# Kernel optimization log

Hardware: AMD Instinct MI355X
Metric: run time of the kernel (lower is better)

The kernel has to match this reference:

```python
import jax, jax.numpy as jnp
import numpy as np

N_NODES = 50000
NEG_SLOPE = 0.2  # PyG GATConv default
DROP_P = 0.3


def gat_layer(x, src, dst, W, a_src, a_dst, b, n):
    # x: [N, din]; src/dst: [E'] (self-loops already appended)
    h = x @ W                                   # [N, dout]
    s_src = (h * a_src).sum(-1)                 # [N]
    s_dst = (h * a_dst).sum(-1)                 # [N]
    alpha = jax.nn.leaky_relu(s_src[src] + s_dst[dst], NEG_SLOPE)  # [E']
    # segment softmax over destination node
    amax = jax.ops.segment_max(alpha, dst, num_segments=n)
    e = jnp.exp(alpha - amax[dst])
    denom = jax.ops.segment_sum(e, dst, num_segments=n)
    coef = e / denom[dst]                       # [E']
    out = jax.ops.segment_sum(coef[:, None] * h[src], dst, num_segments=n)
    return out + b


def setup_inputs() -> dict:
    key = jax.random.key(0)
    ks = jax.random.split(key, 10)
    d1, d2 = 64, 64
    E = jax.random.normal(ks[0], (N_NODES, d1), jnp.float32)
    A = jax.random.randint(ks[1], (2, 800000), 0, N_NODES, jnp.int64)
    W1 = jax.random.normal(ks[2], (d1, d1), jnp.float32) / np.sqrt(d1)
    a_src1 = jax.random.normal(ks[3], (d1,), jnp.float32) / np.sqrt(d1)
    a_dst1 = jax.random.normal(ks[4], (d1,), jnp.float32) / np.sqrt(d1)
    b1 = jnp.zeros((d1,), jnp.float32)
    W2 = jax.random.normal(ks[5], (d1, d2), jnp.float32) / np.sqrt(d1)
    a_src2 = jax.random.normal(ks[6], (d2,), jnp.float32) / np.sqrt(d2)
    a_dst2 = jax.random.normal(ks[7], (d2,), jnp.float32) / np.sqrt(d2)
    b2 = jnp.zeros((d2,), jnp.float32)
    return {"E": E, "A": A, "W1": W1, "a_src1": a_src1, "a_dst1": a_dst1,
            "b1": b1, "W2": W2, "a_src2": a_src2, "a_dst2": a_dst2, "b2": b2}


def reference(E, A, W1, a_src1, a_dst1, b1, W2, a_src2, a_dst2, b2):
    n = E.shape[0]
    loop = jnp.arange(n, dtype=A.dtype)
    src = jnp.concatenate([A[0], loop])  # PyG GATConv adds self-loops
    dst = jnp.concatenate([A[1], loop])
    x1 = jax.nn.relu(gat_layer(E, src, dst, W1, a_src1, a_dst1, b1, n))
    # F.dropout(p=0.3) runs in training mode by default -> deterministic fixed-key mask
    keep = jax.random.bernoulli(jax.random.key(42), 1.0 - DROP_P, x1.shape)
    x1 = jnp.where(keep, x1 / (1.0 - DROP_P), 0.0)
    x2 = jax.nn.relu(gat_layer(x1, src, dst, W2, a_src2, a_dst2, b2, n))
    return x2
```

## Files before the change

### kernel.cpp

```cpp
#include <hip/hip_runtime.h>


__device__ __forceinline__ unsigned rotl32(unsigned x, unsigned r) {
  return (x << r) | (x >> (32u - r));
}

__device__ __forceinline__ void threefry2_0_42(unsigned c0, unsigned c1,
                                               unsigned* o0, unsigned* o1) {
  const unsigned k0 = 0u, k1 = 42u;
  const unsigned k2 = k0 ^ k1 ^ 0x1BD11BDAu;
  unsigned ks[3] = {k0, k1, k2};
  unsigned x0 = c0 + ks[0];
  unsigned x1 = c1 + ks[1];
  const unsigned R[2][4] = {{13u, 15u, 26u, 6u}, {17u, 29u, 16u, 24u}};
#pragma unroll
  for (int i = 0; i < 5; ++i) {
#pragma unroll
    for (int j = 0; j < 4; ++j) {
      unsigned r = R[i & 1][j];
      x0 += x1;
      x1 = rotl32(x1, r);
      x1 ^= x0;
    }
    x0 += ks[(i + 1) % 3];
    x1 += ks[(i + 2) % 3] + (unsigned)(i + 1);
  }
  *o0 = x0;
  *o1 = x1;
}

__device__ __forceinline__ float ldf(const void* p, int isbf, size_t i) {
  if (isbf) {
    unsigned short u = ((const unsigned short*)p)[i];
    return __uint_as_float(((unsigned)u) << 16);
  }
  return ((const float*)p)[i];
}

__global__ __launch_bounds__(256) void k_prep(
    const void* __restrict__ A, const void* __restrict__ Ein, int nNodes,
    const void* W1, const void* as1, const void* ad1, const void* b1,
    const void* W2, const void* as2, const void* ad2, const void* b2,
    float* __restrict__ smallc, int* __restrict__ deg, int* __restrict__ cursor,
    int* __restrict__ flags) {
  __shared__ int s_ok64, s_bf;
  int t = threadIdx.x;
  if (t == 0) { s_ok64 = 1; s_bf = 0; }
  __syncthreads();
  long long v = ((const long long*)A)[t];
  if (!(v >= 0 && v < (long long)nNodes)) atomicAnd(&s_ok64, 0);
  unsigned w = ((const unsigned*)Ein)[t];
  unsigned b = (w >> 8) & 0x7F;
  if (b >= 0x3A && b <= 0x43) atomicAdd(&s_bf, 1);
  __syncthreads();
  int isbf = (s_bf >= 200) ? 1 : 0;
  int i = blockIdx.x * 256 + t;
  if (blockIdx.x == 0 && t == 0) {
    flags[0] = s_ok64;
    flags[1] = isbf;
  }
  if (i < 8576) {
    float x;
    if (i < 4096) x = ldf(W1, isbf, i);
    else if (i < 4160) x = ldf(as1, isbf, i - 4096);
    else if (i < 4224) x = ldf(ad1, isbf, i - 4160);
    else if (i < 4288) x = ldf(b1, isbf, i - 4224);
    else if (i < 8384) x = ldf(W2, isbf, i - 4288);
    else if (i < 8448) x = ldf(as2, isbf, i - 8384);
    else if (i < 8512) x = ldf(ad2, isbf, i - 8448);
    else x = ldf(b2, isbf, i - 8512);
    smallc[i] = x;
  }
  if (i < nNodes) {
    deg[i] = 1;
    cursor[i] = 0;
  }
}

__global__ __launch_bounds__(256) void k_count_gemm(
    const void* __restrict__ A, const int* __restrict__ flags, int Eb,
    int* __restrict__ deg, const void* __restrict__ X,
    const float* __restrict__ W, const float* __restrict__ a_src,
    const float* __restrict__ a_dst, float* __restrict__ H,
    float* __restrict__ ssrc, float* __restrict__ sdst, int n,
    int nCountBlocks) {
  __shared__ float Wl[64 * 64];
  int t = threadIdx.x;
  if ((int)blockIdx.x < nCountBlocks) {
    int e = blockIdx.x * 256 + t;
    if (e < Eb) {
      int d = flags[0] ? (int)((const long long*)A)[(long long)Eb + e]
                       : ((const int*)A)[Eb + e];
      atomicAdd(&deg[d], 1);
    }
    return;
  }
  int bid = blockIdx.x - nCountBlocks;
  for (int i = t; i < 64 * 64; i += 256) Wl[i] = W[i];
  __syncthreads();
  int lane = t & 63;
  int row = bid * 4 + (t >> 6);
  if (row >= n) return;
  int isbf = flags[1];
  float xv = ldf(X, isbf, (size_t)row * 64 + lane);
  float acc = 0.f;
#pragma unroll
  for (int k = 0; k < 64; ++k) {
    float xk = __shfl(xv, k);
    acc = fmaf(xk, Wl[k * 64 + lane], acc);
  }
  H[(size_t)row * 64 + lane] = acc;
  float vs = acc * a_src[lane];
  float vd = acc * a_dst[lane];
#pragma unroll
  for (int d = 32; d; d >>= 1) {
    vs += __shfl_xor(vs, d);
    vd += __shfl_xor(vd, d);
  }
  if (lane == 0) {
    ssrc[row] = vs;
    sdst[row] = vd;
  }
}

__global__ __launch_bounds__(256) void k_gemm64(
    const float* __restrict__ X, const float* __restrict__ W,
    const float* __restrict__ a_src, const float* __restrict__ a_dst,
    float* __restrict__ H, float* __restrict__ ssrc, float* __restrict__ sdst,
    int n) {
  __shared__ float Wl[64 * 64];
  int t = threadIdx.x;
  for (int i = t; i < 64 * 64; i += 256) Wl[i] = W[i];
  __syncthreads();
  int lane = t & 63;
  int row = blockIdx.x * 4 + (t >> 6);
  if (row >= n) return;
  float xv = X[(size_t)row * 64 + lane];
  float acc = 0.f;
#pragma unroll
  for (int k = 0; k < 64; ++k) {
    float xk = __shfl(xv, k);
    acc = fmaf(xk, Wl[k * 64 + lane], acc);
  }
  H[(size_t)row * 64 + lane] = acc;
  float vs = acc * a_src[lane];
  float vd = acc * a_dst[lane];
#pragma unroll
  for (int d = 32; d; d >>= 1) {
    vs += __shfl_xor(vs, d);
    vd += __shfl_xor(vd, d);
  }
  if (lane == 0) {
    ssrc[row] = vs;
    sdst[row] = vd;
  }
}

__global__ __launch_bounds__(1024) void k_scan_one(const int* __restrict__ deg,
                                                   int* __restrict__ offsets,
                                                   int n, int etot) {
  __shared__ int wsum[16];
  __shared__ int carry;
  int t = threadIdx.x;
  int lane = t & 63;
  int w = t >> 6;
  if (t == 0) carry = 0;
  __syncthreads();
  for (int base = 0; base < n; base += 1024) {
    int i = base + t;
    int x = (i < n) ? deg[i] : 0;
    int sc = x;
#pragma unroll
    for (int d = 1; d < 64; d <<= 1) {
      int o = __shfl_up(sc, d);
      if (lane >= d) sc += o;
    }
    if (lane == 63) wsum[w] = sc;
    __syncthreads();
    int cbase = carry;
    if (t < 64) {
      int v = (t < 16) ? wsum[t] : 0;
#pragma unroll
      for (int d = 1; d < 16; d <<= 1) {
        int o = __shfl_up(v, d);
        if (lane >= d) v += o;
      }
      if (t < 16) wsum[t] = v;
    }
    __syncthreads();
    int wpre = (w == 0) ? 0 : wsum[w - 1];
    if (i < n) offsets[i] = cbase + wpre + (sc - x);
    int tot = wsum[15];
    __syncthreads();
    if (t == 0) carry = cbase + tot;
    __syncthreads();
  }
  if (t == 0) offsets[n] = etot;
}

__global__ __launch_bounds__(256) void k_fill(const void* __restrict__ A,
                                              const int* __restrict__ flags,
                                              const int* __restrict__ offsets,
                                              int* cursor, int* __restrict__ csr,
                                              int Eb, int nnode) {
  int e = blockIdx.x * 256 + threadIdx.x;
  if (e >= Eb + nnode) return;
  int s, d;
  if (e < Eb) {
    if (flags[0]) {
      s = (int)((const long long*)A)[e];
      d = (int)((const long long*)A)[(long long)Eb + e];
    } else {
      s = ((const int*)A)[e];
      d = ((const int*)A)[Eb + e];
    }
  } else {
    s = d = e - Eb;
  }
  int slot = atomicAdd(&cursor[d], 1);
  csr[offsets[d] + slot] = s;
}

#define AGG_STEP(IDX, ACC)                                              \
  {                                                                     \
    int idx_ = (IDX);                                                   \
    float cl_ = __shfl(c, idx_);                                        \
    int sr_ = __shfl(sl, idx_);                                         \
    if (idx_ < glim) {                                                  \
      const float4 hv_ = *(const float4*)&h[(size_t)sr_ * 64 + f4 * 4]; \
      ACC.x = fmaf(cl_, hv_.x, ACC.x);                                  \
      ACC.y = fmaf(cl_, hv_.y, ACC.y);                                  \
      ACC.z = fmaf(cl_, hv_.z, ACC.z);                                  \
      ACC.w = fmaf(cl_, hv_.w, ACC.w);                                  \
    }                                                                   \
  }

template <int DROPOUT>
__global__ __launch_bounds__(256) void k_aggregate(
    const float* __restrict__ h, const float* __restrict__ ssrc,
    const float* __restrict__ sdst, const float* __restrict__ bias,
    const int* __restrict__ offsets, const int* __restrict__ csr,
    float* __restrict__ alphaE, float* __restrict__ out, int n) {
  int wid = (blockIdx.x * 256 + threadIdx.x) >> 6;
  int lane = threadIdx.x & 63;
  if (wid >= n) return;
  int off = offsets[wid];
  int end = offsets[wid + 1];
  int g = end - off;
  float sd = sdst[wid];
  int e4 = lane >> 4, f4 = lane & 15;
  float4 acc0 = {0.f, 0.f, 0.f, 0.f}, acc1 = {0.f, 0.f, 0.f, 0.f};

  if (g <= 64) {
    int sl = 0;
    float v = -1e30f;
    if (lane < g) {
      sl = csr[off + lane];
      float tv = ssrc[sl] + sd;
      v = (tv > 0.f) ? tv : 0.2f * tv;
    }
    float m = v;
#pragma unroll
    for (int d = 32; d; d >>= 1) m = fmaxf(m, __shfl_xor(m, d));
    float ex = (lane < g) ? __expf(v - m) : 0.f;
    float s = ex;
#pragma unroll
    for (int d = 32; d; d >>= 1) s += __shfl_xor(s, d);
    float c = ex * (1.f / s);
    int glim = g;
    for (int cb = 0; cb < g; cb += 8) {
      AGG_STEP(cb + e4, acc0)
      AGG_STEP(cb + 4 + e4, acc1)
    }
  } else {
    float mm = -1e30f, ss = 0.f;
    for (int e = off + lane; e < end; e += 64) {
      int sl2 = csr[e];
      float tv = ssrc[sl2] + sd;
      tv = (tv > 0.f) ? tv : 0.2f * tv;
      alphaE[e] = tv;
      float mn = fmaxf(mm, tv);
      ss = ss * __expf(mm - mn) + __expf(tv - mn);
      mm = mn;
    }
#pragma unroll
    for (int d = 32; d; d >>= 1) {
      float mo = __shfl_xor(mm, d);
      float so = __shfl_xor(ss, d);
      float mn = fmaxf(mm, mo);
      ss = ss * __expf(mm - mn) + so * __expf(mo - mn);
      mm = mn;
    }
    float inv = 1.f / ss;
    for (int base = off; base < end; base += 64) {
      int e = base + lane;
      int cnt = min(64, end - base);
      float c = 0.f;
      int sl = 0;
      if (e < end) {
        c = __expf(alphaE[e] - mm) * inv;
        sl = csr[e];
      }
      int glim = cnt;
      for (int cb = 0; cb < cnt; cb += 8) {
        AGG_STEP(cb + e4, acc0)
        AGG_STEP(cb + 4 + e4, acc1)
      }
    }
  }

  float4 r;
  r.x = acc0.x + acc1.x;
  r.y = acc0.y + acc1.y;
  r.z = acc0.z + acc1.z;
  r.w = acc0.w + acc1.w;
#pragma unroll
  for (int d = 16; d < 64; d <<= 1) {
    r.x += __shfl_xor(r.x, d);
    r.y += __shfl_xor(r.y, d);
    r.z += __shfl_xor(r.z, d);
    r.w += __shfl_xor(r.w, d);
  }

  unsigned long long mask = 0ull;
  if (DROPOUT) {
    unsigned i0 = (unsigned)wid * 64u + (unsigned)lane;
    unsigned o0, o1;
    threefry2_0_42(0u, i0, &o0, &o1);
    unsigned bits = o0 ^ o1;
    float u = __uint_as_float((bits >> 9) | 0x3f800000u) - 1.0f;
    mask = __ballot(u < 0.7f);
  }

  if (lane < 16) {
    const float4 b4 = *(const float4*)&bias[lane * 4];
    r.x = fmaxf(r.x + b4.x, 0.f);
    r.y = fmaxf(r.y + b4.y, 0.f);
    r.z = fmaxf(r.z + b4.z, 0.f);
    r.w = fmaxf(r.w + b4.w, 0.f);
    if (DROPOUT) {
      r.x = ((mask >> (lane * 4 + 0)) & 1ull) ? r.x / 0.7f : 0.f;
      r.y = ((mask >> (lane * 4 + 1)) & 1ull) ? r.y / 0.7f : 0.f;
      r.z = ((mask >> (lane * 4 + 2)) & 1ull) ? r.z / 0.7f : 0.f;
      r.w = ((mask >> (lane * 4 + 3)) & 1ull) ? r.w / 0.7f : 0.f;
    }
    *(float4*)&out[(size_t)wid * 64 + lane * 4] = r;
  }
}

extern "C" void kernel_launch(void* const* d_in, const int* in_sizes, int n_in,
                              void* d_out, int out_size, void* d_ws, size_t ws_size,
                              hipStream_t stream) {
  const void* E = d_in[0];
  const void* A = d_in[1];
  const void* W1 = d_in[2];
  const void* as1 = d_in[3];
  const void* ad1 = d_in[4];
  const void* b1 = d_in[5];
  const void* W2 = d_in[6];
  const void* as2 = d_in[7];
  const void* ad2 = d_in[8];
  const void* b2 = d_in[9];
  float* out = (float*)d_out;

  const int N = in_sizes[0] / 64;
  const int Eb = in_sizes[1] / 2;
  const int Etot = Eb + N;
  const int total = N * 64;

  float* ws = (float*)d_ws;
  float* h = ws;
  float* x1 = h + (size_t)total;
  float* ssrc = x1 + (size_t)total;
  float* sdst = ssrc + N;
  float* alphaE = sdst + N;
  float* smallc = alphaE + Etot;
  int* deg = (int*)(smallc + 8576);
  int* offsets = deg + N;
  int* cursor = offsets + (N + 1);
  int* flags = cursor + N;
  int* csr = flags + 2;

  float* W1c = smallc;
  float* as1c = smallc + 4096;
  float* ad1c = smallc + 4160;
  float* b1c = smallc + 4224;
  float* W2c = smallc + 4288;
  float* as2c = smallc + 8384;
  float* ad2c = smallc + 8448;
  float* b2c = smallc + 8512;

  const int gPrep = (N + 255) / 256;
  const int nCountBlocks = (Eb + 255) / 256;
  const int gGemm = (N + 3) / 4;
  const int gFill = (Etot + 255) / 256;

  k_prep<<<gPrep, 256, 0, stream>>>(A, E, N, W1, as1, ad1, b1, W2, as2, ad2,
                                    b2, smallc, deg, cursor, flags);
  k_count_gemm<<<nCountBlocks + gGemm, 256, 0, stream>>>(
      A, flags, Eb, deg, E, W1c, as1c, ad1c, h, ssrc, sdst, N, nCountBlocks);
  k_scan_one<<<1, 1024, 0, stream>>>(deg, offsets, N, Etot);
  k_fill<<<gFill, 256, 0, stream>>>(A, flags, offsets, cursor, csr, Eb, N);
  k_aggregate<1><<<gGemm, 256, 0, stream>>>(h, ssrc, sdst, b1c, offsets, csr,
                                            alphaE, x1, N);
  k_gemm64<<<gGemm, 256, 0, stream>>>(x1, W2c, as2c, ad2c, h, ssrc, sdst, N);
  k_aggregate<0><<<gGemm, 256, 0, stream>>>(h, ssrc, sdst, b2c, offsets, csr,
                                            alphaE, out, N);
}
```

Before: 396.4 us.

## Use register-tiled 64x64 GEMM with transposed X in shared memory

Replaces the per-row shuffle-based GEMM, one wavefront per row, with a 64-row tile per block. X is staged transposed in padded LDS and each thread computes a 4x4 output block using float4 loads from shared memory. The attention scores are reduced with 16-lane shuffles. The separate second-layer GEMM kernel is removed, and the second layer reuses the combined kernel with zero count blocks. This cuts shared-memory traffic per FMA and raises arithmetic intensity, at the cost of more LDS per block and a transposed scatter on load.

```diff
diff --git a/kernel.cpp b/kernel.cpp
--- a/kernel.cpp
+++ b/kernel.cpp
@@ -1,5 +1,7 @@
 #include <hip/hip_runtime.h>
 
+
+#define XT_STRIDE 68
 
 __device__ __forceinline__ unsigned rotl32(unsigned x, unsigned r) {
   return (x << r) | (x >> (32u - r));
@@ -79,12 +81,13 @@
 
 __global__ __launch_bounds__(256) void k_count_gemm(
     const void* __restrict__ A, const int* __restrict__ flags, int Eb,
-    int* __restrict__ deg, const void* __restrict__ X,
+    int* __restrict__ deg, const void* __restrict__ X, int xDetect,
     const float* __restrict__ W, const float* __restrict__ a_src,
     const float* __restrict__ a_dst, float* __restrict__ H,
     float* __restrict__ ssrc, float* __restrict__ sdst, int n,
     int nCountBlocks) {
-  __shared__ float Wl[64 * 64];
+  __shared__ float Xt[64 * XT_STRIDE];
+  __shared__ float Ws[64 * 64];
   int t = threadIdx.x;
   if ((int)blockIdx.x < nCountBlocks) {
     int e = blockIdx.x * 256 + t;
@@ -96,63 +99,83 @@
     return;
   }
   int bid = blockIdx.x - nCountBlocks;
-  for (int i = t; i < 64 * 64; i += 256) Wl[i] = W[i];
+  int row0 = bid * 64;
+  int isbf = xDetect ? flags[1] : 0;
+
+#pragma unroll
+  for (int i = t; i < 1024; i += 256) {
+    int k = i >> 4, jq = i & 15;
+    *(float4*)&Ws[k * 64 + jq * 4] = *(const float4*)&W[k * 64 + jq * 4];
+  }
+#pragma unroll
+  for (int i = t; i < 1024; i += 256) {
+    int q = i & 15, r = i >> 4;
+    int row = row0 + r;
+    float4 v = {0.f, 0.f, 0.f, 0.f};
+    if (row < n) {
+      if (isbf) {
+        v.x = ldf(X, 1, (size_t)row * 64 + q * 4 + 0);
+        v.y = ldf(X, 1, (size_t)row * 64 + q * 4 + 1);
+        v.z = ldf(X, 1, (size_t)row * 64 + q * 4 + 2);
+        v.w = ldf(X, 1, (size_t)row * 64 + q * 4 + 3);
+      } else {
+        v = *(const float4*)&((const float*)X)[(size_t)row * 64 + q * 4];
+      }
+    }
+    Xt[(q * 4 + 0) * XT_STRIDE + r] = v.x;
+    Xt[(q * 4 + 1) * XT_STRIDE + r] = v.y;
+    Xt[(q * 4 + 2) * XT_STRIDE + r] = v.z;
+    Xt[(q * 4 + 3) * XT_STRIDE + r] = v.w;
+  }
   __syncthreads();
-  int lane = t & 63;
-  int row = bid * 4 + (t >> 6);
-  if (row >= n) return;
-  int isbf = flags[1];
-  float xv = ldf(X, isbf, (size_t)row * 64 + lane);
-  float acc = 0.f;
-#pragma unroll
+
+  int r0 = (t >> 4) * 4;
+  int c0 = (t & 15) * 4;
+  float acc[4][4];
+#pragma unroll
+  for (int r = 0; r < 4; ++r)
+#pragma unroll
+    for (int c = 0; c < 4; ++c) acc[r][c] = 0.f;
+
+#pragma unroll 8
   for (int k = 0; k < 64; ++k) {
-    float xk = __shfl(xv, k);
-    acc = fmaf(xk, Wl[k * 64 + lane], acc);
-  }
-  H[(size_t)row * 64 + lane] = acc;
-  float vs = acc * a_src[lane];
-  float vd = acc * a_dst[lane];
-#pragma unroll
-  for (int d = 32; d; d >>= 1) {
-    vs += __shfl_xor(vs, d);
-    vd += __shfl_xor(vd, d);
-  }
-  if (lane == 0) {
-    ssrc[row] = vs;
-    sdst[row] = vd;
-  }
-}
-
-__global__ __launch_bounds__(256) void k_gemm64(
-    const float* __restrict__ X, const float* __restrict__ W,
-    const float* __restrict__ a_src, const float* __restrict__ a_dst,
-    float* __restrict__ H, float* __restrict__ ssrc, float* __restrict__ sdst,
-    int n) {
-  __shared__ float Wl[64 * 64];
-  int t = threadIdx.x;
-  for (int i = t; i < 64 * 64; i += 256) Wl[i] = W[i];
-  __syncthreads();
-  int lane = t & 63;
-  int row = blockIdx.x * 4 + (t >> 6);
-  if (row >= n) return;
-  float xv = X[(size_t)row * 64 + lane];
-  float acc = 0.f;
-#pragma unroll
-  for (int k = 0; k < 64; ++k) {
-    float xk = __shfl(xv, k);
-    acc = fmaf(xk, Wl[k * 64 + lane], acc);
-  }
-  H[(size_t)row * 64 + lane] = acc;
-  float vs = acc * a_src[lane];
-  float vd = acc * a_dst[lane];
-#pragma unroll
-  for (int d = 32; d; d >>= 1) {
-    vs += __shfl_xor(vs, d);
-    vd += __shfl_xor(vd, d);
-  }
-  if (lane == 0) {
-    ssrc[row] = vs;
-    sdst[row] = vd;
+    float4 a4 = *(const float4*)&Xt[k * XT_STRIDE + r0];
+    float4 b4 = *(const float4*)&Ws[k * 64 + c0];
+    const float av[4] = {a4.x, a4.y, a4.z, a4.w};
+    const float bv[4] = {b4.x, b4.y, b4.z, b4.w};
+#pragma unroll
+    for (int r = 0; r < 4; ++r)
+#pragma unroll
+      for (int c = 0; c < 4; ++c) acc[r][c] = fmaf(av[r], bv[c], acc[r][c]);
+  }
+
+  const float4 asr = *(const float4*)&a_src[c0];
+  const float4 adr = *(const float4*)&a_dst[c0];
+#pragma unroll
+  for (int r = 0; r < 4; ++r) {
+    float vs = acc[r][0] * asr.x + acc[r][1] * asr.y + acc[r][2] * asr.z +
+               acc[r][3] * asr.w;
+    float vd = acc[r][0] * adr.x + acc[r][1] * adr.y + acc[r][2] * adr.z +
+               acc[r][3] * adr.w;
+#pragma unroll
+    for (int d = 1; d < 16; d <<= 1) {
+      vs += __shfl_xor(vs, d);
+      vd += __shfl_xor(vd, d);
+    }
+    int row = row0 + r0 + r;
+    if ((t & 15) == 0 && row < n) {
+      ssrc[row] = vs;
+      sdst[row] = vd;
+    }
+  }
+
+#pragma unroll
+  for (int r = 0; r < 4; ++r) {
+    int row = row0 + r0 + r;
+    if (row < n) {
+      float4 o = {acc[r][0], acc[r][1], acc[r][2], acc[r][3]};
+      *(float4*)&H[(size_t)row * 64 + c0] = o;
+    }
   }
 }
 
@@ -392,18 +415,20 @@
 
   const int gPrep = (N + 255) / 256;
   const int nCountBlocks = (Eb + 255) / 256;
-  const int gGemm = (N + 3) / 4;
+  const int gTile = (N + 63) / 64;
+  const int gAgg = (N + 3) / 4;
   const int gFill = (Etot + 255) / 256;
 
   k_prep<<<gPrep, 256, 0, stream>>>(A, E, N, W1, as1, ad1, b1, W2, as2, ad2,
                                     b2, smallc, deg, cursor, flags);
-  k_count_gemm<<<nCountBlocks + gGemm, 256, 0, stream>>>(
-      A, flags, Eb, deg, E, W1c, as1c, ad1c, h, ssrc, sdst, N, nCountBlocks);
+  k_count_gemm<<<nCountBlocks + gTile, 256, 0, stream>>>(
+      A, flags, Eb, deg, E, 1, W1c, as1c, ad1c, h, ssrc, sdst, N, nCountBlocks);
   k_scan_one<<<1, 1024, 0, stream>>>(deg, offsets, N, Etot);
   k_fill<<<gFill, 256, 0, stream>>>(A, flags, offsets, cursor, csr, Eb, N);
-  k_aggregate<1><<<gGemm, 256, 0, stream>>>(h, ssrc, sdst, b1c, offsets, csr,
-                                            alphaE, x1, N);
-  k_gemm64<<<gGemm, 256, 0, stream>>>(x1, W2c, as2c, ad2c, h, ssrc, sdst, N);
-  k_aggregate<0><<<gGemm, 256, 0, stream>>>(h, ssrc, sdst, b2c, offsets, csr,
-                                            alphaE, out, N);
-}
+  k_aggregate<1><<<gAgg, 256, 0, stream>>>(h, ssrc, sdst, b1c, offsets, csr,
+                                           alphaE, x1, N);
+  k_count_gemm<<<gTile, 256, 0, stream>>>(A, flags, Eb, deg, x1, 0, W2c, as2c,
+                                          ad2c, h, ssrc, sdst, N, 0);
+  k_aggregate<0><<<gAgg, 256, 0, stream>>>(h, ssrc, sdst, b2c, offsets, csr,
+                                           alphaE, out, N);
+}
```

After: 320.5 us. 19.1% less time.
